# Kernel optimization log

Measured on AMD Instinct MI355X. Metric: run time of the kernel, lower is better.

## Reference

```python
import jax, jax.numpy as jnp
import numpy as np


def setup_inputs() -> dict:
    key = jax.random.key(0)
    k1, k2, k3 = jax.random.split(key, 3)
    B, C, H, W = 8, 128, 128, 128
    kh, kw = 5, 5
    x = jax.random.normal(k1, (B, C, H, W), dtype=jnp.float32)
    weight = jax.random.normal(k2, (B, C, kh, kw), dtype=jnp.float32)
    bias = jax.random.normal(k3, (B, C), dtype=jnp.float32)
    return {"x": x, "weight": weight, "bias": bias, "padding": 2, "stride": 1}


def reference(x, weight, bias, padding, stride):
    # Morphological dilation with external SE: out = max_k(x_patch + w_k) + bias.
    # torch unfold zero-pads, so padded zeros legitimately participate in the max-plus.
    B, C, H, W = x.shape
    kh, kw = weight.shape[-2:]
    ph = pw = int(padding)
    sh = sw = int(stride)
    H2 = (H + 2 * ph - kh) // sh + 1
    W2 = (W + 2 * pw - kw) // sw + 1
    xp = jnp.pad(x, ((0, 0), (0, 0), (ph, ph), (pw, pw)))
    y = None
    # Fixed small kh*kw loop; each iter is a vectorized shifted-window max-plus.
    for di in range(kh):
        for dj in range(kw):
            patch = xp[:, :, di:di + sh * H2:sh, dj:dj + sw * W2:sw]  # B,C,H2,W2
            val = patch + weight[:, :, di, dj][:, :, None, None]
            y = val if y is None else jnp.maximum(y, val)
    return y + bias[:, :, None, None]
```

## Files before the change

kernel.cpp:

```cpp
#include <hip/hip_runtime.h>


static constexpr int H = 128, W = 128, KH = 5, KW = 5, PAD = 2;
static constexpr int QROWS = 32;
static constexpr int PROWS = QROWS + KH - 1;
static constexpr int PCOLS = W + 2 * PAD;
static constexpr int NQ    = H / QROWS;

#define MAX3(a, b, c) fmaxf(fmaxf((a), (b)), (c))

__device__ inline void gload_lds4(const float* g, float* l) {
    __builtin_amdgcn_global_load_lds(
        (const __attribute__((address_space(1))) void*)g,
        (__attribute__((address_space(3))) void*)l, 4, 0, 0);
}

__global__ __launch_bounds__(256) void dilation_kernel(
    const float* __restrict__ x,
    const float* __restrict__ wgt,
    const float* __restrict__ bias,
    float* __restrict__ out)
{
    __shared__ float tile[PROWS * PCOLS];

    const int plane = blockIdx.x / NQ;
    const int q     = blockIdx.x % NQ;
    const int tid   = threadIdx.x;

    const float* __restrict__ xp = x   + (size_t)plane * (H * W);
    float*       __restrict__ op = out + (size_t)plane * (H * W);
    const float* __restrict__ wp = wgt + plane * (KH * KW);

    if (tid < 2 * PROWS) {
        const int r   = tid >> 1;
        const int off = (tid & 1) ? (PCOLS - 2) : 0;
        tile[r * PCOLS + off]     = 0.0f;
        tile[r * PCOLS + off + 1] = 0.0f;
    }
    if (q == 0 && tid < PCOLS) {
        tile[tid]         = 0.0f;
        tile[PCOLS + tid] = 0.0f;
    }
    if (q == NQ - 1 && tid < PCOLS) {
        tile[(PROWS - 2) * PCOLS + tid] = 0.0f;
        tile[(PROWS - 1) * PCOLS + tid] = 0.0f;
    }

    const int wave = tid >> 6;
    const int lane = tid & 63;
    const int row0 = q * QROWS - PAD;
#pragma unroll
    for (int chunk = 0; chunk < 2 * PROWS; chunk += 4) {
        const int ch   = chunk + wave;
        const int pr   = ch >> 1;
        const int half = (ch & 1) * 64;
        const int irow = row0 + pr;
        if (irow >= 0 && irow < H) {
            gload_lds4(xp + irow * W + half + lane,
                       &tile[pr * PCOLS + PAD + half]);
        }
    }

    __syncthreads();

    float wk[KH * KW];
#pragma unroll
    for (int i = 0; i < KH * KW; ++i) wk[i] = wp[i];
    const float bi = bias[plane];

    const int cg = tid & 31;
    const int rs = tid >> 5;
    const int j0 = cg * 4;
    const int tb = rs * 4;

    float win[KH][8];

#define LOAD_TROW(SLOT, PR)                                                   \
    do {                                                                      \
        const float* rp_ = &tile[(PR) * PCOLS + j0];                          \
        const float4 a_ = *reinterpret_cast<const float4*>(rp_);              \
        const float4 b_ = *reinterpret_cast<const float4*>(rp_ + 4);          \
        win[SLOT][0] = a_.x; win[SLOT][1] = a_.y;                             \
        win[SLOT][2] = a_.z; win[SLOT][3] = a_.w;                             \
        win[SLOT][4] = b_.x; win[SLOT][5] = b_.y;                             \
        win[SLOT][6] = b_.z; win[SLOT][7] = b_.w;                             \
    } while (0)

#pragma unroll
    for (int t = 0; t < KH - 1; ++t)
        LOAD_TROW(t, tb + t);

#pragma unroll
    for (int it = 0; it < 4; ++it) {
        LOAD_TROW((it + KH - 1) % KH, tb + it + KH - 1);

        float res[4];
#pragma unroll
        for (int k = 0; k < 4; ++k) {
            float v[KH * KW];
#pragma unroll
            for (int r = 0; r < KH; ++r) {
                const int s = (it + r) % KH;
#pragma unroll
                for (int c = 0; c < KW; ++c)
                    v[r * KW + c] = win[s][k + c] + wk[r * KW + c];
            }
            const float u0 = MAX3(v[0],  v[1],  v[2]);
            const float u1 = MAX3(v[3],  v[4],  v[5]);
            const float u2 = MAX3(v[6],  v[7],  v[8]);
            const float u3 = MAX3(v[9],  v[10], v[11]);
            const float u4 = MAX3(v[12], v[13], v[14]);
            const float u5 = MAX3(v[15], v[16], v[17]);
            const float u6 = MAX3(v[18], v[19], v[20]);
            const float u7 = MAX3(v[21], v[22], v[23]);
            const float w0 = MAX3(u0, u1, u2);
            const float w1 = MAX3(u3, u4, u5);
            const float w2 = MAX3(u6, u7, v[24]);
            res[k] = MAX3(w0, w1, w2) + bi;
        }

        float4 o;
        o.x = res[0]; o.y = res[1]; o.z = res[2]; o.w = res[3];
        const int grow = q * QROWS + tb + it;
        *reinterpret_cast<float4*>(op + grow * W + j0) = o;
    }
#undef LOAD_TROW
}

extern "C" void kernel_launch(void* const* d_in, const int* in_sizes, int n_in,
                              void* d_out, int out_size, void* d_ws, size_t ws_size,
                              hipStream_t stream) {
    const float* x    = (const float*)d_in[0];
    const float* wgt  = (const float*)d_in[1];
    const float* bias = (const float*)d_in[2];
    float* out        = (float*)d_out;

    const int planes = in_sizes[2];
    dim3 grid(planes * NQ);
    dim3 block(256);
    dilation_kernel<<<grid, block, 0, stream>>>(x, wgt, bias, out);
}
```

Measured before the change: 122.5 us.

## Process whole plane per block with double-buffered LDS prefetch of row tiles

Each block now handles one entire plane instead of a quarter. It loops over four row tiles and uses two LDS buffers, so the async global-to-LDS load of the next tile is issued while the current tile is being computed. The goal is to hide global load latency and to zero the padding once per plane. In exchange the grid shrinks fourfold, to 1024 blocks, and LDS use per block doubles, which cuts the number of resident blocks and the parallelism available to hide latency.

```diff
diff --git a/kernel.cpp b/kernel.cpp
--- a/kernel.cpp
+++ b/kernel.cpp
@@ -2,10 +2,10 @@
 
 
 static constexpr int H = 128, W = 128, KH = 5, KW = 5, PAD = 2;
-static constexpr int QROWS = 32;
-static constexpr int PROWS = QROWS + KH - 1;
+static constexpr int TROWS = 32;
+static constexpr int PROWS = TROWS + KH - 1;
 static constexpr int PCOLS = W + 2 * PAD;
-static constexpr int NQ    = H / QROWS;
+static constexpr int NT    = H / TROWS;
 
 #define MAX3(a, b, c) fmaxf(fmaxf((a), (b)), (c))
 
@@ -21,47 +21,46 @@
     const float* __restrict__ bias,
     float* __restrict__ out)
 {
-    __shared__ float tile[PROWS * PCOLS];
+    __shared__ float tile[2][PROWS * PCOLS];
 
-    const int plane = blockIdx.x / NQ;
-    const int q     = blockIdx.x % NQ;
+    const int plane = blockIdx.x;
     const int tid   = threadIdx.x;
+    const int wave  = tid >> 6;
+    const int lane  = tid & 63;
 
     const float* __restrict__ xp = x   + (size_t)plane * (H * W);
     float*       __restrict__ op = out + (size_t)plane * (H * W);
     const float* __restrict__ wp = wgt + plane * (KH * KW);
 
-    if (tid < 2 * PROWS) {
-        const int r   = tid >> 1;
-        const int off = (tid & 1) ? (PCOLS - 2) : 0;
-        tile[r * PCOLS + off]     = 0.0f;
-        tile[r * PCOLS + off + 1] = 0.0f;
+#define STAGE(BUF, T)                                                         \
+    do {                                                                      \
+        const int r0_ = (T) * TROWS - PAD;                                    \
+        _Pragma("unroll")                                                     \
+        for (int chunk = 0; chunk < 2 * PROWS; chunk += 4) {                  \
+            const int ch   = chunk + wave;                  \
+            const int pr   = ch >> 1;                                         \
+            const int half = (ch & 1) * 64;                                   \
+            const int irow = r0_ + pr;                                        \
+            if (irow >= 0 && irow < H)                                        \
+                gload_lds4(xp + irow * W + half + lane,                       \
+                           &tile[BUF][pr * PCOLS + PAD + half]);              \
+        }                                                                     \
+    } while (0)
+
+    STAGE(0, 0);
+
+    if (tid < 144) {
+        const int b  = tid / 72;
+        const int r2 = tid % 72;
+        const int r  = r2 >> 1;
+        const int off = (r2 & 1) ? (PCOLS - 2) : 0;
+        tile[b][r * PCOLS + off]     = 0.0f;
+        tile[b][r * PCOLS + off + 1] = 0.0f;
     }
-    if (q == 0 && tid < PCOLS) {
-        tile[tid]         = 0.0f;
-        tile[PCOLS + tid] = 0.0f;
+    if (tid < PCOLS) {
+        tile[0][tid]         = 0.0f;
+        tile[0][PCOLS + tid] = 0.0f;
     }
-    if (q == NQ - 1 && tid < PCOLS) {
-        tile[(PROWS - 2) * PCOLS + tid] = 0.0f;
-        tile[(PROWS - 1) * PCOLS + tid] = 0.0f;
-    }
-
-    const int wave = tid >> 6;
-    const int lane = tid & 63;
-    const int row0 = q * QROWS - PAD;
-#pragma unroll
-    for (int chunk = 0; chunk < 2 * PROWS; chunk += 4) {
-        const int ch   = chunk + wave;
-        const int pr   = ch >> 1;
-        const int half = (ch & 1) * 64;
-        const int irow = row0 + pr;
-        if (irow >= 0 && irow < H) {
-            gload_lds4(xp + irow * W + half + lane,
-                       &tile[pr * PCOLS + PAD + half]);
-        }
-    }
-
-    __syncthreads();
 
     float wk[KH * KW];
 #pragma unroll
@@ -73,58 +72,75 @@
     const int j0 = cg * 4;
     const int tb = rs * 4;
 
-    float win[KH][8];
-
-#define LOAD_TROW(SLOT, PR)                                                   \
-    do {                                                                      \
-        const float* rp_ = &tile[(PR) * PCOLS + j0];                          \
-        const float4 a_ = *reinterpret_cast<const float4*>(rp_);              \
-        const float4 b_ = *reinterpret_cast<const float4*>(rp_ + 4);          \
-        win[SLOT][0] = a_.x; win[SLOT][1] = a_.y;                             \
-        win[SLOT][2] = a_.z; win[SLOT][3] = a_.w;                             \
-        win[SLOT][4] = b_.x; win[SLOT][5] = b_.y;                             \
-        win[SLOT][6] = b_.z; win[SLOT][7] = b_.w;                             \
-    } while (0)
+    __syncthreads();
 
 #pragma unroll
-    for (int t = 0; t < KH - 1; ++t)
-        LOAD_TROW(t, tb + t);
+    for (int t = 0; t < NT; ++t) {
+        const int cur = t & 1;
+
+        if (t < NT - 1) STAGE(cur ^ 1, t + 1);
+        if (t == 2 && tid < PCOLS) {
+            tile[1][(PROWS - 2) * PCOLS + tid] = 0.0f;
+            tile[1][(PROWS - 1) * PCOLS + tid] = 0.0f;
+        }
+
+        const float* __restrict__ tp = tile[cur];
+
+        float win[KH][8];
+#define LOAD_TROW(SLOT, PR)                                                   \
+        do {                                                                  \
+            const float* rp_ = tp + (PR) * PCOLS + j0;                        \
+            const float4 a_ = *reinterpret_cast<const float4*>(rp_);          \
+            const float4 b_ = *reinterpret_cast<const float4*>(rp_ + 4);      \
+            win[SLOT][0] = a_.x; win[SLOT][1] = a_.y;                         \
+            win[SLOT][2] = a_.z; win[SLOT][3] = a_.w;                         \
+            win[SLOT][4] = b_.x; win[SLOT][5] = b_.y;                         \
+            win[SLOT][6] = b_.z; win[SLOT][7] = b_.w;                         \
+        } while (0)
 
 #pragma unroll
-    for (int it = 0; it < 4; ++it) {
-        LOAD_TROW((it + KH - 1) % KH, tb + it + KH - 1);
+        for (int pt = 0; pt < KH - 1; ++pt)
+            LOAD_TROW(pt, tb + pt);
 
-        float res[4];
 #pragma unroll
-        for (int k = 0; k < 4; ++k) {
-            float v[KH * KW];
+        for (int it = 0; it < 4; ++it) {
+            LOAD_TROW((it + KH - 1) % KH, tb + it + KH - 1);
+
+            float res[4];
 #pragma unroll
-            for (int r = 0; r < KH; ++r) {
-                const int s = (it + r) % KH;
+            for (int k = 0; k < 4; ++k) {
+                float v[KH * KW];
 #pragma unroll
-                for (int c = 0; c < KW; ++c)
-                    v[r * KW + c] = win[s][k + c] + wk[r * KW + c];
+                for (int r = 0; r < KH; ++r) {
+                    const int s = (it + r) % KH;
+#pragma unroll
+                    for (int c = 0; c < KW; ++c)
+                        v[r * KW + c] = win[s][k + c] + wk[r * KW + c];
+                }
+                const float u0 = MAX3(v[0],  v[1],  v[2]);
+                const float u1 = MAX3(v[3],  v[4],  v[5]);
+                const float u2 = MAX3(v[6],  v[7],  v[8]);
+                const float u3 = MAX3(v[9],  v[10], v[11]);
+                const float u4 = MAX3(v[12], v[13], v[14]);
+                const float u5 = MAX3(v[15], v[16], v[17]);
+                const float u6 = MAX3(v[18], v[19], v[20]);
+                const float u7 = MAX3(v[21], v[22], v[23]);
+                const float w0 = MAX3(u0, u1, u2);
+                const float w1 = MAX3(u3, u4, u5);
+                const float w2 = MAX3(u6, u7, v[24]);
+                res[k] = MAX3(w0, w1, w2) + bi;
             }
-            const float u0 = MAX3(v[0],  v[1],  v[2]);
-            const float u1 = MAX3(v[3],  v[4],  v[5]);
-            const float u2 = MAX3(v[6],  v[7],  v[8]);
-            const float u3 = MAX3(v[9],  v[10], v[11]);
-            const float u4 = MAX3(v[12], v[13], v[14]);
-            const float u5 = MAX3(v[15], v[16], v[17]);
-            const float u6 = MAX3(v[18], v[19], v[20]);
-            const float u7 = MAX3(v[21], v[22], v[23]);
-            const float w0 = MAX3(u0, u1, u2);
-            const float w1 = MAX3(u3, u4, u5);
-            const float w2 = MAX3(u6, u7, v[24]);
-            res[k] = MAX3(w0, w1, w2) + bi;
+
+            float4 o;
+            o.x = res[0]; o.y = res[1]; o.z = res[2]; o.w = res[3];
+            const int grow = t * TROWS + tb + it;
+            *reinterpret_cast<float4*>(op + grow * W + j0) = o;
         }
+#undef LOAD_TROW
 
-        float4 o;
-        o.x = res[0]; o.y = res[1]; o.z = res[2]; o.w = res[3];
-        const int grow = q * QROWS + tb + it;
-        *reinterpret_cast<float4*>(op + grow * W + j0) = o;
+        __syncthreads();
     }
-#undef LOAD_TROW
+#undef STAGE
 }
 
 extern "C" void kernel_launch(void* const* d_in, const int* in_sizes, int n_in,
@@ -136,7 +152,7 @@
     float* out        = (float*)d_out;
 
     const int planes = in_sizes[2];
-    dim3 grid(planes * NQ);
+    dim3 grid(planes);
     dim3 block(256);
     dilation_kernel<<<grid, block, 0, stream>>>(x, wgt, bias, out);
 }
```

New measurement: 125.2 us. 2.2% more time.
